# Optimization experiments

Hardware: AMD Instinct MI355X
Metric: run time of the kernel (lower is better)

The kernel has to match this reference:

```python
import jax, jax.numpy as jnp
import numpy as np

N_QUBITS = 4
INV_SQRT2 = np.float32(1.0 / np.sqrt(2.0))
CNOT_PAIRS = [(0, 1), (1, 2), (2, 3), (3, 0), (0, 2), (1, 3), (2, 0), (3, 1)]


def _apply_1q(state, U, w):
    # state: (B,2,2,2,2); U: (B,2,2) batched or (2,2) shared
    state = jnp.moveaxis(state, w + 1, 1)
    if U.ndim == 3:
        state = jnp.einsum('bij,bj...->bi...', U, state)
    else:
        state = jnp.einsum('ij,bj...->bi...', U, state)
    return jnp.moveaxis(state, 1, w + 1)


def _apply_cnot(state, c, t):
    st = jnp.moveaxis(state, (c + 1, t + 1), (1, 2))
    st = jnp.stack([st[:, 0], st[:, 1, ::-1]], axis=1)  # flip target where ctrl=1
    return jnp.moveaxis(st, (1, 2), (c + 1, t + 1))


def _ry_batched(theta):  # theta: (B,) -> (B,2,2) complex
    c, s = jnp.cos(theta * 0.5), jnp.sin(theta * 0.5)
    return jnp.stack([jnp.stack([c, -s], -1), jnp.stack([s, c], -1)], -2).astype(jnp.complex64)


def _rz_batched(theta):  # theta: (B,) -> (B,2,2) complex (diag(e^{-i t/2}, e^{i t/2}))
    e = jnp.exp(-0.5j * theta.astype(jnp.complex64))
    z = jnp.zeros_like(e)
    return jnp.stack([jnp.stack([e, z], -1), jnp.stack([z, jnp.conj(e)], -1)], -2)


def _ry1(t):  # scalar -> (2,2)
    c, s = jnp.cos(t * 0.5), jnp.sin(t * 0.5)
    return jnp.stack([jnp.stack([c, -s]), jnp.stack([s, c])]).astype(jnp.complex64)


def _rz1(t):  # scalar -> (2,2)
    e = jnp.exp(-0.5j * t.astype(jnp.complex64))
    z = jnp.zeros_like(e)
    return jnp.stack([jnp.stack([e, z]), jnp.stack([z, jnp.conj(e)])])


def _circuit(f, weights):
    # f: (B, 4) angle features; weights: (L, 4, 3). Returns <Z_i> per wire: (B, 4).
    B = f.shape[0]
    state = jnp.zeros((B, 2, 2, 2, 2), jnp.complex64).at[:, 0, 0, 0, 0].set(1.0)
    H = jnp.array([[1.0, 1.0], [1.0, -1.0]], jnp.complex64) * INV_SQRT2
    for i in range(N_QUBITS):
        state = _apply_1q(state, H, i)
        state = _apply_1q(state, _ry_batched(jnp.arctan(f[:, i])), i)
        state = _apply_1q(state, _rz_batched(jnp.arctan(f[:, i] ** 2)), i)
    n_layers = weights.shape[0]
    for l in range(n_layers):
        for c, t in CNOT_PAIRS:
            state = _apply_cnot(state, c, t)
        for i in range(N_QUBITS):
            phi, theta, omega = weights[l, i, 0], weights[l, i, 1], weights[l, i, 2]
            # PennyLane Rot(phi, theta, omega) = RZ(omega) @ RY(theta) @ RZ(phi)
            U = _rz1(omega) @ _ry1(theta) @ _rz1(phi)
            state = _apply_1q(state, U, i)
    probs = jnp.abs(state) ** 2  # (B,2,2,2,2)
    z = []
    for i in range(N_QUBITS):
        axes = tuple(a for a in range(1, N_QUBITS + 1) if a != i + 1)
        m = probs.sum(axes)  # (B,2)
        z.append(m[:, 0] - m[:, 1])
    return jnp.stack(z, -1)


def setup_inputs() -> dict:
    key = jax.random.key(0)
    ks = jax.random.split(key, 6)
    B, D_IN, D_OUT, L = 131072, 256, 64, 2
    x = jax.random.normal(ks[0], (B, D_IN), jnp.float32)
    W1 = jax.random.normal(ks[1], (N_QUBITS, D_IN), jnp.float32) * (1.0 / np.sqrt(D_IN))
    b1 = jax.random.normal(ks[2], (N_QUBITS,), jnp.float32) * 0.1
    weights = jax.random.normal(ks[3], (L, N_QUBITS, 3), jnp.float32)
    W2 = jax.random.normal(ks[4], (D_OUT, N_QUBITS), jnp.float32) * 0.5
    b2 = jax.random.normal(ks[5], (D_OUT,), jnp.float32) * 0.1
    return {"x": x, "W1": W1, "b1": b1, "weights": weights, "W2": W2, "b2": b2}


def reference(x, W1, b1, weights, W2, b2):
    f = jnp.tanh(x @ W1.T + b1) * jnp.pi  # (B,4)
    q = _circuit(f, weights)              # (B,4) expval(PauliZ)
    return q @ W2.T + b2                  # (B, D_OUT)
```

## Files before the change

### kernel.cpp

```cpp
#include <hip/hip_runtime.h>
#include <math.h>

#define NQ 4
#define DIN 256
#define DOUT 64
#define NLAYER 2
#define TPB 256
#define BROWS 64

__device__ __forceinline__ float tanh_fast(float y) {
    float e = __expf(2.0f * y);
    return 1.0f - 2.0f / (e + 1.0f);
}

__global__ __launch_bounds__(TPB, 4) void qp_fused(
    const float* __restrict__ x,  const float* __restrict__ W1,
    const float* __restrict__ b1, const float* __restrict__ wts,
    const float* __restrict__ W2, const float* __restrict__ b2,
    float* __restrict__ out)
{
    __shared__ __align__(16) float fs[BROWS][NQ];
    __shared__ __align__(16) float qs[BROWS][NQ];
    __shared__ __align__(16) float w2s[DOUT][NQ];
    __shared__ __align__(16) float us[8][8];
    __shared__ float b2s[DOUT];

    const int t = threadIdx.x;
    const int wave = t >> 6, lane = t & 63;
    const int rsub = lane >> 4;
    const int cc   = lane & 15;
    const int brow = blockIdx.x * BROWS;

    if (t < 64) {
        ((float4*)&w2s[0][0])[t] = ((const float4*)W2)[t];
        b2s[t] = b2[t];
    }
    if (t < 8) {
        const float phi = wts[t*3 + 0], th = wts[t*3 + 1], om = wts[t*3 + 2];
        float sth, cth; sincosf(0.5f*th, &sth, &cth);
        float sp, cp;   sincosf(0.5f*(phi+om), &sp, &cp);
        float sm, cm;   sincosf(0.5f*(phi-om), &sm, &cm);
        us[t][0] =  cth*cp; us[t][1] = -cth*sp;
        us[t][2] = -sth*cm; us[t][3] = -sth*sm;
        us[t][4] =  sth*cm; us[t][5] = -sth*sm;
        us[t][6] =  cth*cp; us[t][7] =  cth*sp;
    }

    {
        float4 w[4][4];
        #pragma unroll
        for (int q = 0; q < 4; ++q)
            #pragma unroll
            for (int p = 0; p < 4; ++p)
                w[q][p] = ((const float4*)W1)[q*64 + p*16 + cc];
        const float4 bv = *(const float4*)b1;

        const int rowbase = brow + wave*4 + rsub;
        const float4* xr0 = (const float4*)(x + (size_t)rowbase * DIN);

        float4 xv0 = xr0[cc], xv1 = xr0[16+cc], xv2 = xr0[32+cc], xv3 = xr0[48+cc];
        #pragma unroll
        for (int it = 0; it < BROWS/16; ++it) {
            float4 nv0, nv1, nv2, nv3;
            if (it < BROWS/16 - 1) {
                const float4* xr = (const float4*)(x + (size_t)(rowbase + (it+1)*16) * DIN);
                nv0 = xr[cc]; nv1 = xr[16+cc]; nv2 = xr[32+cc]; nv3 = xr[48+cc];
            }
            float a0=0.f, a1=0.f, a2=0.f, a3=0.f;
            #pragma unroll
            for (int p = 0; p < 4; ++p) {
                const float4 xv = (p==0)?xv0:(p==1)?xv1:(p==2)?xv2:xv3;
                a0 = fmaf(xv.x,w[0][p].x, fmaf(xv.y,w[0][p].y, fmaf(xv.z,w[0][p].z, fmaf(xv.w,w[0][p].w, a0))));
                a1 = fmaf(xv.x,w[1][p].x, fmaf(xv.y,w[1][p].y, fmaf(xv.z,w[1][p].z, fmaf(xv.w,w[1][p].w, a1))));
                a2 = fmaf(xv.x,w[2][p].x, fmaf(xv.y,w[2][p].y, fmaf(xv.z,w[2][p].z, fmaf(xv.w,w[2][p].w, a2))));
                a3 = fmaf(xv.x,w[3][p].x, fmaf(xv.y,w[3][p].y, fmaf(xv.z,w[3][p].z, fmaf(xv.w,w[3][p].w, a3))));
            }
            #pragma unroll
            for (int d = 1; d < 16; d <<= 1) {
                a0 += __shfl_xor(a0, d, 64);
                a1 += __shfl_xor(a1, d, 64);
                a2 += __shfl_xor(a2, d, 64);
                a3 += __shfl_xor(a3, d, 64);
            }
            if (cc == 0) {
                const float PI = 3.14159265358979f;
                const int rloc = it*16 + wave*4 + rsub;
                float4 o;
                o.x = PI * tanh_fast(a0 + bv.x);
                o.y = PI * tanh_fast(a1 + bv.y);
                o.z = PI * tanh_fast(a2 + bv.z);
                o.w = PI * tanh_fast(a3 + bv.w);
                *(float4*)&fs[rloc][0] = o;
            }
            xv0 = nv0; xv1 = nv1; xv2 = nv2; xv3 = nv3;
        }
    }
    __syncthreads();

    if (t < BROWS) {
        const float4 fv = ((const float4*)fs)[t];
        const float fq[4] = {fv.x, fv.y, fv.z, fv.w};
        const float IS2 = 0.70710678118654752f;
        float vr[4][2], vi[4][2];
        #pragma unroll
        for (int i = 0; i < 4; ++i) {
            const float fi = fq[i];
            const float f2 = fi*fi;
            const float ca = rsqrtf(1.0f + f2);
            const float ch = sqrtf(0.5f*(1.0f + ca));
            const float sh = copysignf(sqrtf(fmaxf(0.5f*(1.0f - ca), 0.0f)), fi);
            const float cb = rsqrtf(1.0f + f2*f2);
            const float cbh = sqrtf(0.5f*(1.0f + cb));
            const float sbh = sqrtf(fmaxf(0.5f*(1.0f - cb), 0.0f));
            const float u0 = (ch - sh) * IS2;
            const float u1 = (ch + sh) * IS2;
            vr[i][0] = u0 * cbh;  vi[i][0] = -u0 * sbh;
            vr[i][1] = u1 * cbh;  vi[i][1] =  u1 * sbh;
        }
        float ar[16], ai[16];
        #pragma unroll
        for (int i0 = 0; i0 < 2; ++i0)
        #pragma unroll
        for (int i1 = 0; i1 < 2; ++i1) {
            const float pr  = vr[0][i0]*vr[1][i1] - vi[0][i0]*vi[1][i1];
            const float pim = vr[0][i0]*vi[1][i1] + vi[0][i0]*vr[1][i1];
            #pragma unroll
            for (int i2 = 0; i2 < 2; ++i2)
            #pragma unroll
            for (int i3 = 0; i3 < 2; ++i3) {
                const float qr  = vr[2][i2]*vr[3][i3] - vi[2][i2]*vi[3][i3];
                const float qim = vr[2][i2]*vi[3][i3] + vi[2][i2]*vr[3][i3];
                const int idx = i0*8 + i1*4 + i2*2 + i3;
                ar[idx] = pr*qr - pim*qim;
                ai[idx] = pr*qim + pim*qr;
            }
        }
        #pragma unroll
        for (int l = 0; l < NLAYER; ++l) {
            constexpr int cpairs[8][2] = {{0,1},{1,2},{2,3},{3,0},{0,2},{1,3},{2,0},{3,1}};
            #pragma unroll
            for (int g = 0; g < 8; ++g) {
                const int bc = 8 >> cpairs[g][0];
                const int bt = 8 >> cpairs[g][1];
                #pragma unroll
                for (int m = 0; m < 16; ++m) {
                    if ((m & bc) && !(m & bt)) {
                        const int m2 = m | bt;
                        float tr = ar[m]; ar[m] = ar[m2]; ar[m2] = tr;
                        float ti = ai[m]; ai[m] = ai[m2]; ai[m2] = ti;
                    }
                }
            }
            #pragma unroll
            for (int i = 0; i < 4; ++i) {
                const float* u = &us[l*4 + i][0];
                const float u00r=u[0], u00i=u[1], u01r=u[2], u01i=u[3];
                const float u10r=u[4], u10i=u[5], u11r=u[6], u11i=u[7];
                const int bq = 8 >> i;
                #pragma unroll
                for (int m = 0; m < 16; ++m) {
                    if (!(m & bq)) {
                        const int m2 = m | bq;
                        const float a0r=ar[m], a0i=ai[m], a1r=ar[m2], a1i=ai[m2];
                        ar[m]  = u00r*a0r - u00i*a0i + u01r*a1r - u01i*a1i;
                        ai[m]  = u00r*a0i + u00i*a0r + u01r*a1i + u01i*a1r;
                        ar[m2] = u10r*a0r - u10i*a0i + u11r*a1r - u11i*a1i;
                        ai[m2] = u10r*a0i + u10i*a0r + u11r*a1i + u11i*a1r;
                    }
                }
            }
        }
        float z0=0.f, z1=0.f, z2=0.f, z3=0.f;
        #pragma unroll
        for (int m = 0; m < 16; ++m) {
            const float p = ar[m]*ar[m] + ai[m]*ai[m];
            z0 += (m & 8) ? -p : p;
            z1 += (m & 4) ? -p : p;
            z2 += (m & 2) ? -p : p;
            z3 += (m & 1) ? -p : p;
        }
        float4 qv; qv.x=z0; qv.y=z1; qv.z=z2; qv.w=z3;
        ((float4*)qs)[t] = qv;
    }
    __syncthreads();

    {
        const int j4 = t & 15;
        const int rb = t >> 4;
        float w2r[4][4], b2r[4];
        #pragma unroll
        for (int jj = 0; jj < 4; ++jj) {
            const int j = j4*4 + jj;
            #pragma unroll
            for (int i = 0; i < 4; ++i) w2r[jj][i] = w2s[j][i];
            b2r[jj] = b2s[j];
        }
        #pragma unroll
        for (int e = 0; e < 4; ++e) {
            const int r = rb*4 + e;
            const float4 q = ((const float4*)qs)[r];
            float4 o;
            o.x = fmaf(q.x,w2r[0][0], fmaf(q.y,w2r[0][1], fmaf(q.z,w2r[0][2], fmaf(q.w,w2r[0][3], b2r[0]))));
            o.y = fmaf(q.x,w2r[1][0], fmaf(q.y,w2r[1][1], fmaf(q.z,w2r[1][2], fmaf(q.w,w2r[1][3], b2r[1]))));
            o.z = fmaf(q.x,w2r[2][0], fmaf(q.y,w2r[2][1], fmaf(q.z,w2r[2][2], fmaf(q.w,w2r[2][3], b2r[2]))));
            o.w = fmaf(q.x,w2r[3][0], fmaf(q.y,w2r[3][1], fmaf(q.z,w2r[3][2], fmaf(q.w,w2r[3][3], b2r[3]))));
            ((float4*)(out + (size_t)(brow + r) * DOUT))[j4] = o;
        }
    }
}

extern "C" void kernel_launch(void* const* d_in, const int* in_sizes, int n_in,
                              void* d_out, int out_size, void* d_ws, size_t ws_size,
                              hipStream_t stream) {
    const float* x  = (const float*)d_in[0];
    const float* W1 = (const float*)d_in[1];
    const float* b1 = (const float*)d_in[2];
    const float* wt = (const float*)d_in[3];
    const float* W2 = (const float*)d_in[4];
    const float* b2 = (const float*)d_in[5];
    float* out = (float*)d_out;
    const int B = in_sizes[0] / DIN;
    qp_fused<<<B / BROWS, TPB, 0, stream>>>(x, W1, b1, wt, W2, b2, out);
}
```

Before: 43.56 us.

## Use 32 lanes per row with reduce-scatter shuffles and double rows per block

The projection stage now gives each input row to 32 lanes instead of 16. The four dot-product partials are reduced in two xor-shuffle steps, then each lane keeps one of the four outputs and finishes it with three more shuffles, a reduce-scatter pattern that cuts total shuffle count. Rows per block double to 128, so each block covers more of the batch and the per-block setup (W1/W2 loads, rotation matrices) is amortised over more rows. The trade-off is fewer bytes of x in flight per thread and half as many blocks, which may reduce latency hiding on a mostly memory-bound kernel.

```diff
diff --git a/kernel.cpp b/kernel.cpp
--- a/kernel.cpp
+++ b/kernel.cpp
@@ -6,7 +6,7 @@
 #define DOUT 64
 #define NLAYER 2
 #define TPB 256
-#define BROWS 64
+#define BROWS 128
 
 __device__ __forceinline__ float tanh_fast(float y) {
     float e = __expf(2.0f * y);
@@ -27,8 +27,8 @@
 
     const int t = threadIdx.x;
     const int wave = t >> 6, lane = t & 63;
-    const int rsub = lane >> 4;
-    const int cc   = lane & 15;
+    const int half = lane >> 5;
+    const int cl   = lane & 31;
     const int brow = blockIdx.x * BROWS;
 
     if (t < 64) {
@@ -47,52 +47,51 @@
     }
 
     {
-        float4 w[4][4];
-        #pragma unroll
-        for (int q = 0; q < 4; ++q)
-            #pragma unroll
-            for (int p = 0; p < 4; ++p)
-                w[q][p] = ((const float4*)W1)[q*64 + p*16 + cc];
+        float4 w[4][2];
+        #pragma unroll
+        for (int q = 0; q < 4; ++q) {
+            w[q][0] = ((const float4*)W1)[q*64 + cl];
+            w[q][1] = ((const float4*)W1)[q*64 + 32 + cl];
+        }
         const float4 bv = *(const float4*)b1;
-
-        const int rowbase = brow + wave*4 + rsub;
-        const float4* xr0 = (const float4*)(x + (size_t)rowbase * DIN);
-
-        float4 xv0 = xr0[cc], xv1 = xr0[16+cc], xv2 = xr0[32+cc], xv3 = xr0[48+cc];
-        #pragma unroll
-        for (int it = 0; it < BROWS/16; ++it) {
-            float4 nv0, nv1, nv2, nv3;
-            if (it < BROWS/16 - 1) {
-                const float4* xr = (const float4*)(x + (size_t)(rowbase + (it+1)*16) * DIN);
-                nv0 = xr[cc]; nv1 = xr[16+cc]; nv2 = xr[32+cc]; nv3 = xr[48+cc];
-            }
-            float a0=0.f, a1=0.f, a2=0.f, a3=0.f;
-            #pragma unroll
-            for (int p = 0; p < 4; ++p) {
-                const float4 xv = (p==0)?xv0:(p==1)?xv1:(p==2)?xv2:xv3;
-                a0 = fmaf(xv.x,w[0][p].x, fmaf(xv.y,w[0][p].y, fmaf(xv.z,w[0][p].z, fmaf(xv.w,w[0][p].w, a0))));
-                a1 = fmaf(xv.x,w[1][p].x, fmaf(xv.y,w[1][p].y, fmaf(xv.z,w[1][p].z, fmaf(xv.w,w[1][p].w, a1))));
-                a2 = fmaf(xv.x,w[2][p].x, fmaf(xv.y,w[2][p].y, fmaf(xv.z,w[2][p].z, fmaf(xv.w,w[2][p].w, a2))));
-                a3 = fmaf(xv.x,w[3][p].x, fmaf(xv.y,w[3][p].y, fmaf(xv.z,w[3][p].z, fmaf(xv.w,w[3][p].w, a3))));
-            }
-            #pragma unroll
-            for (int d = 1; d < 16; d <<= 1) {
-                a0 += __shfl_xor(a0, d, 64);
-                a1 += __shfl_xor(a1, d, 64);
-                a2 += __shfl_xor(a2, d, 64);
-                a3 += __shfl_xor(a3, d, 64);
-            }
-            if (cc == 0) {
+        const int qsel = lane & 3;
+        const float bsel = (qsel==0)?bv.x:(qsel==1)?bv.y:(qsel==2)?bv.z:bv.w;
+
+        const int row0 = brow + wave*2 + half;
+        const float4* xr = (const float4*)(x + (size_t)row0 * DIN);
+        float4 xv0 = xr[cl], xv1 = xr[32 + cl];
+
+        #pragma unroll
+        for (int it = 0; it < BROWS/8; ++it) {
+            float4 nv0, nv1;
+            if (it < BROWS/8 - 1) {
+                const float4* xn = (const float4*)(x + (size_t)(row0 + (it+1)*8) * DIN);
+                nv0 = xn[cl]; nv1 = xn[32 + cl];
+            }
+            float a0, a1, a2, a3;
+            a0 = fmaf(xv0.x,w[0][0].x, fmaf(xv0.y,w[0][0].y, fmaf(xv0.z,w[0][0].z, xv0.w*w[0][0].w)));
+            a1 = fmaf(xv0.x,w[1][0].x, fmaf(xv0.y,w[1][0].y, fmaf(xv0.z,w[1][0].z, xv0.w*w[1][0].w)));
+            a2 = fmaf(xv0.x,w[2][0].x, fmaf(xv0.y,w[2][0].y, fmaf(xv0.z,w[2][0].z, xv0.w*w[2][0].w)));
+            a3 = fmaf(xv0.x,w[3][0].x, fmaf(xv0.y,w[3][0].y, fmaf(xv0.z,w[3][0].z, xv0.w*w[3][0].w)));
+            a0 = fmaf(xv1.x,w[0][1].x, fmaf(xv1.y,w[0][1].y, fmaf(xv1.z,w[0][1].z, fmaf(xv1.w,w[0][1].w, a0))));
+            a1 = fmaf(xv1.x,w[1][1].x, fmaf(xv1.y,w[1][1].y, fmaf(xv1.z,w[1][1].z, fmaf(xv1.w,w[1][1].w, a1))));
+            a2 = fmaf(xv1.x,w[2][1].x, fmaf(xv1.y,w[2][1].y, fmaf(xv1.z,w[2][1].z, fmaf(xv1.w,w[2][1].w, a2))));
+            a3 = fmaf(xv1.x,w[3][1].x, fmaf(xv1.y,w[3][1].y, fmaf(xv1.z,w[3][1].z, fmaf(xv1.w,w[3][1].w, a3))));
+
+            a0 += __shfl_xor(a0, 1, 64);  a1 += __shfl_xor(a1, 1, 64);
+            a2 += __shfl_xor(a2, 1, 64);  a3 += __shfl_xor(a3, 1, 64);
+            a0 += __shfl_xor(a0, 2, 64);  a1 += __shfl_xor(a1, 2, 64);
+            a2 += __shfl_xor(a2, 2, 64);  a3 += __shfl_xor(a3, 2, 64);
+            float v = (qsel==0)?a0:(qsel==1)?a1:(qsel==2)?a2:a3;
+            v += __shfl_xor(v, 4, 64);
+            v += __shfl_xor(v, 8, 64);
+            v += __shfl_xor(v, 16, 64);
+
+            if (cl < 4) {
                 const float PI = 3.14159265358979f;
-                const int rloc = it*16 + wave*4 + rsub;
-                float4 o;
-                o.x = PI * tanh_fast(a0 + bv.x);
-                o.y = PI * tanh_fast(a1 + bv.y);
-                o.z = PI * tanh_fast(a2 + bv.z);
-                o.w = PI * tanh_fast(a3 + bv.w);
-                *(float4*)&fs[rloc][0] = o;
-            }
-            xv0 = nv0; xv1 = nv1; xv2 = nv2; xv3 = nv3;
+                fs[it*8 + wave*2 + half][qsel] = PI * tanh_fast(v + bsel);
+            }
+            xv0 = nv0; xv1 = nv1;
         }
     }
     __syncthreads();
@@ -196,8 +195,8 @@
             b2r[jj] = b2s[j];
         }
         #pragma unroll
-        for (int e = 0; e < 4; ++e) {
-            const int r = rb*4 + e;
+        for (int e = 0; e < BROWS/16; ++e) {
+            const int r = rb*(BROWS/16) + e;
             const float4 q = ((const float4*)qs)[r];
             float4 o;
             o.x = fmaf(q.x,w2r[0][0], fmaf(q.y,w2r[0][1], fmaf(q.z,w2r[0][2], fmaf(q.w,w2r[0][3], b2r[0]))));
```

Measured after the change: 39.80 us. 8.6% less time.
